# Kernel tuning notes

Measured on AMD Instinct MI355X. Metric: run time of the kernel, lower is better.

## Reference

```python
import jax, jax.numpy as jnp
import numpy as np

HIDDEN = 1024
HEADS = 16


def rotate_half(x):
    x1, x2 = jnp.split(x, 2, axis=-1)
    return jnp.concatenate((-x2, x1), axis=-1)


def rope_tables(seq_len, dim):
    inv_freq = 1.0 / 10000 ** (jnp.arange(0, dim, 2, dtype=jnp.float32) / dim)
    t = jnp.arange(seq_len, dtype=jnp.float32)
    freqs = jnp.outer(t, inv_freq)
    emb = jnp.concatenate((freqs, freqs), axis=-1)  # [S, dim]
    return jnp.cos(emb), jnp.sin(emb)


def setup_inputs() -> dict:
    key = jax.random.key(0)
    ks = jax.random.split(key, 10)
    B, S, D = 2, 2048, HIDDEN
    scale = 1.0 / np.sqrt(D)
    inp = {
        "inputs": jax.random.normal(ks[0], (B, S, D), jnp.float32),
        "context": jax.random.normal(ks[1], (B, S, D), jnp.float32),
        "Wq": jax.random.normal(ks[2], (D, D), jnp.float32) * scale,
        "bq": jnp.zeros((D,), jnp.float32),
        "Wk": jax.random.normal(ks[3], (D, D), jnp.float32) * scale,
        "bk": jnp.zeros((D,), jnp.float32),
        "Wv": jax.random.normal(ks[4], (D, D), jnp.float32) * scale,
        "bv": jnp.zeros((D,), jnp.float32),
        "Wo": jax.random.normal(ks[5], (D, D), jnp.float32) * scale,
        "bo": jnp.zeros((D,), jnp.float32),
    }
    return inp


def reference(inputs, context, Wq, bq, Wk, bk, Wv, bv, Wo, bo):
    B, S, D = inputs.shape
    H = HEADS
    hd = D // H

    q = inputs @ Wq + bq          # [B,S,D]
    k = context @ Wk + bk
    v = context @ Wv + bv

    # RoPE applied over the FULL hidden dim, pre-head-split (faithful to source).
    cos, sin = rope_tables(S, D)  # [S,D]
    # source indexes [0] after broadcasting with [1,1,S,D] tables -> effectively same values
    q = q * cos + rotate_half(q) * sin
    k = k * cos + rotate_half(k) * sin

    q = q.reshape(B, S, H, hd)
    k = k.reshape(B, S, H, hd)
    v = v.reshape(B, S, H, hd)

    # Faithful: NO transpose before attention; matmul contracts last dims of
    # q [B,S,H,hd] with k^T [B,S,hd,H] -> scores [B,S,H,H]
    scores = jnp.einsum('bshd,btd->bsht', q, jnp.zeros((1, 1, 1))) if False else None
    scores = jnp.matmul(q, jnp.swapaxes(k, -2, -1)) / jnp.sqrt(jnp.float32(hd))  # [B,S,H,H]
    attn = jax.nn.softmax(scores, axis=-1)
    ctx = jnp.matmul(attn, v)     # [B,S,H,hd]

    # source: transpose(0,2,1,3) then reshape back to (B,S,D)
    ctx = ctx.transpose(0, 2, 1, 3).reshape(B, S, D)
    out = ctx @ Wo + bo
    return out, attn
```

## Files before the change

kernel.cpp:

```cpp
#include <hip/hip_runtime.h>
#include <hip/hip_bf16.h>
#include <cstdint>

typedef __attribute__((ext_vector_type(8))) short short8;
typedef __attribute__((ext_vector_type(4))) float f32x4;
typedef __attribute__((ext_vector_type(4))) float float4v;
typedef __attribute__((ext_vector_type(4))) unsigned short us4;

#define HD 1024
#define SEQ 2048

__device__ __forceinline__ unsigned short f2bf(float f) {
  uint32_t u = __builtin_bit_cast(uint32_t, f);
  return (unsigned short)((u + 0x7FFFu + ((u >> 16) & 1u)) >> 16);
}
__device__ __forceinline__ float bf2f(unsigned short s) {
  return __builtin_bit_cast(float, (uint32_t)s << 16);
}

__device__ __forceinline__ void gload16(const unsigned short* g, unsigned short* l) {
  __builtin_amdgcn_global_load_lds(
      (const __attribute__((address_space(1))) void*)g,
      (__attribute__((address_space(3))) void*)l, 16, 0, 0);
}

__global__ __launch_bounds__(256) void prep(
    const float* __restrict__ X, const float* __restrict__ Y,
    const float* __restrict__ w0, const float* __restrict__ w1,
    const float* __restrict__ w2, const float* __restrict__ w3,
    unsigned short* __restrict__ Xh, unsigned short* __restrict__ Yh,
    unsigned short* __restrict__ wt) {
  __shared__ float tile[32][33];
  int bx = blockIdx.x;
  int tid = threadIdx.x;
  if (bx < 4096) {
    const float* src = (bx >= 2048) ? Y : X;
    unsigned short* oh = (bx >= 2048) ? Yh : Xh;
    int i0 = (bx & 2047) * 512 + tid;
#pragma unroll
    for (int r = 0; r < 2; ++r) {
      int i = i0 + r * 256;
      float4v v = ((const float4v*)src)[i];
      us4 h;
#pragma unroll
      for (int j = 0; j < 4; ++j) h[j] = f2bf(v[j]);
      ((us4*)oh)[i] = h;
    }
  } else {
    int t = bx - 4096;
    int z = t >> 10;
    int rem = t & 1023;
    int bxx = rem & 31, byy = rem >> 5;
    const float* in = (z == 0) ? w0 : (z == 1) ? w1 : (z == 2) ? w2 : w3;
    unsigned short* oh = wt + (size_t)z * 1024 * 1024;
    int tx = tid & 31, ty = tid >> 5;
    int x = bxx * 32 + tx;
    int y0 = byy * 32;
    for (int i = ty; i < 32; i += 8)
      tile[i][tx] = in[(size_t)(y0 + i) * HD + x];
    __syncthreads();
    int x2 = y0 + tx;
    int y2 = bxx * 32;
    for (int i = ty; i < 32; i += 8)
      oh[(size_t)(y2 + i) * HD + x2] = f2bf(tile[tx][i]);
  }
}

__global__ __launch_bounds__(256, 3) void gemm_qkv(
    const unsigned short* __restrict__ Ih, const unsigned short* __restrict__ Ch,
    const unsigned short* __restrict__ wt,
    const float* __restrict__ bq, const float* __restrict__ bk, const float* __restrict__ bv,
    unsigned short* __restrict__ qo, unsigned short* __restrict__ ko,
    unsigned short* __restrict__ vo) {
  __shared__ __align__(16) unsigned short lds[2][128][64];
  const int K = HD, N = HD;
  const size_t P = (size_t)1024 * 1024;
  int z  = blockIdx.z;
  const unsigned short* Ah = z ? Ch : Ih;
  const unsigned short* Bth = wt + (size_t)z * P;
  const float* bias = (z == 0) ? bq : (z == 1) ? bk : bv;
  unsigned short* C = (z == 0) ? qo : (z == 1) ? ko : vo;

  int m0 = blockIdx.x * 128;
  int n0 = blockIdx.y * 128;
  int tid  = threadIdx.x;
  int lane = tid & 63;
  int w    = tid >> 6;
  int quad = lane >> 4;
  int l16  = lane & 15;
  int wm = (w >> 1) * 64;
  int wn = (w & 1) * 64;

  int ro = lane >> 3;
  int sl = lane & 7;
  int ge = sl ^ (ro >> 1);
  int go = ge ^ 4;
  const unsigned short* spA_e = Ah  + (size_t)(m0 + ro) * K + ge * 8;
  const unsigned short* spA_o = Ah  + (size_t)(m0 + ro) * K + go * 8;
  const unsigned short* spB_e = Bth + (size_t)(n0 + ro) * K + ge * 8;
  const unsigned short* spB_o = Bth + (size_t)(n0 + ro) * K + go * 8;

  f32x4 acc[4][4];
#pragma unroll
  for (int t = 0; t < 4; ++t)
#pragma unroll
    for (int u = 0; u < 4; ++u) acc[t][u] = (f32x4){0.f, 0.f, 0.f, 0.f};

  for (int k0 = 0; k0 < K; k0 += 64) {
    __syncthreads();
#pragma unroll
    for (int i = 0; i < 4; ++i) {
      int seg = w + i * 4;
      const unsigned short* pa = (seg & 1) ? spA_o : spA_e;
      const unsigned short* pb = (seg & 1) ? spB_o : spB_e;
      gload16(pa + (size_t)seg * 8 * K + k0, &lds[0][seg * 8][0]);
      gload16(pb + (size_t)seg * 8 * K + k0, &lds[1][seg * 8][0]);
    }
    __syncthreads();

#pragma unroll
    for (int j = 0; j < 2; ++j) {
      int sl8 = (((j << 2) | quad) ^ (l16 >> 1)) * 8;
      short8 ah[4], bh[4];
#pragma unroll
      for (int t = 0; t < 4; ++t)
        ah[t] = *(const short8*)&lds[0][wm + t * 16 + l16][sl8];
#pragma unroll
      for (int u = 0; u < 4; ++u)
        bh[u] = *(const short8*)&lds[1][wn + u * 16 + l16][sl8];
#pragma unroll
      for (int t = 0; t < 4; ++t)
#pragma unroll
        for (int u = 0; u < 4; ++u)
          acc[t][u] = __builtin_amdgcn_mfma_f32_16x16x32_bf16(ah[t], bh[u], acc[t][u], 0, 0, 0);
    }
  }

#pragma unroll
  for (int t = 0; t < 4; ++t) {
    int row = m0 + wm + t * 16 + quad * 4;
#pragma unroll
    for (int u = 0; u < 4; ++u) {
      int col = n0 + wn + u * 16 + l16;
      float bvv = bias[col];
#pragma unroll
      for (int i = 0; i < 4; ++i)
        C[(size_t)(row + i) * N + col] = f2bf(acc[t][u][i] + bvv);
    }
  }
}

__global__ __launch_bounds__(256, 3) void gemm_o(
    const unsigned short* __restrict__ Ah, const unsigned short* __restrict__ Bth,
    const float* __restrict__ bias, float* __restrict__ C) {
  __shared__ __align__(16) unsigned short ldsA[128][64];
  __shared__ __align__(16) unsigned short ldsB[64][64];
  const int K = HD, N = HD;
  int m0 = blockIdx.x * 128;
  int n0 = blockIdx.y * 64;
  int tid  = threadIdx.x;
  int lane = tid & 63;
  int w    = tid >> 6;
  int quad = lane >> 4;
  int l16  = lane & 15;
  int wm = (w >> 1) * 64;
  int wn = (w & 1) * 32;

  int ro = lane >> 3;
  int sl = lane & 7;
  int ge = sl ^ (ro >> 1);
  int go = ge ^ 4;
  const unsigned short* spA_e = Ah  + (size_t)(m0 + ro) * K + ge * 8;
  const unsigned short* spA_o = Ah  + (size_t)(m0 + ro) * K + go * 8;
  const unsigned short* spB_e = Bth + (size_t)(n0 + ro) * K + ge * 8;
  const unsigned short* spB_o = Bth + (size_t)(n0 + ro) * K + go * 8;

  f32x4 acc[4][2];
#pragma unroll
  for (int t = 0; t < 4; ++t)
#pragma unroll
    for (int u = 0; u < 2; ++u) acc[t][u] = (f32x4){0.f, 0.f, 0.f, 0.f};

  for (int k0 = 0; k0 < K; k0 += 64) {
    __syncthreads();
#pragma unroll
    for (int i = 0; i < 4; ++i) {
      int seg = w + i * 4;
      const unsigned short* pa = (seg & 1) ? spA_o : spA_e;
      gload16(pa + (size_t)seg * 8 * K + k0, &ldsA[seg * 8][0]);
    }
#pragma unroll
    for (int i = 0; i < 2; ++i) {
      int seg = w + i * 4;
      const unsigned short* pb = (seg & 1) ? spB_o : spB_e;
      gload16(pb + (size_t)seg * 8 * K + k0, &ldsB[seg * 8][0]);
    }
    __syncthreads();

#pragma unroll
    for (int j = 0; j < 2; ++j) {
      int sl8 = (((j << 2) | quad) ^ (l16 >> 1)) * 8;
      short8 ah[4], bh[2];
#pragma unroll
      for (int t = 0; t < 4; ++t)
        ah[t] = *(const short8*)&ldsA[wm + t * 16 + l16][sl8];
#pragma unroll
      for (int u = 0; u < 2; ++u)
        bh[u] = *(const short8*)&ldsB[wn + u * 16 + l16][sl8];
#pragma unroll
      for (int t = 0; t < 4; ++t)
#pragma unroll
        for (int u = 0; u < 2; ++u)
          acc[t][u] = __builtin_amdgcn_mfma_f32_16x16x32_bf16(ah[t], bh[u], acc[t][u], 0, 0, 0);
    }
  }

#pragma unroll
  for (int t = 0; t < 4; ++t) {
    int row = m0 + wm + t * 16 + quad * 4;
#pragma unroll
    for (int u = 0; u < 2; ++u) {
      int col = n0 + wn + u * 16 + l16;
      float bvv = bias[col];
#pragma unroll
      for (int i = 0; i < 4; ++i)
        C[(size_t)(row + i) * N + col] = acc[t][u][i] + bvv;
    }
  }
}

__global__ __launch_bounds__(256) void attn_rope_k(
    const unsigned short* __restrict__ q, const unsigned short* __restrict__ kk,
    const unsigned short* __restrict__ v,
    float* __restrict__ attn_out, unsigned short* __restrict__ ctx_h) {
  __shared__ __align__(16) unsigned short vs[4][16][64];
  int tid = threadIdx.x;
  int lane = tid & 63;
  int w = tid >> 6;
  int m = blockIdx.x * 4 + w;
  int s = m & (SEQ - 1);
  int b = m >> 11;
  int l16 = lane & 15;
  int quad = lane >> 4;

  {
    unsigned short* dst = &vs[w][0][0];
    const unsigned short* src = v + (size_t)m * HD;
    gload16(src + lane * 8, dst);
    gload16(src + 512 + lane * 8, dst + 512);
  }

  const unsigned short* qrow = q + (size_t)m * HD + l16 * 64 + quad * 8;
  const unsigned short* krow = kk + (size_t)m * HD + l16 * 64 + quad * 8;
  float qf[2][8], kf[2][8];
#pragma unroll
  for (int j = 0; j < 2; ++j) {
    short8 qv = *(const short8*)(qrow + j * 32);
    short8 kv = *(const short8*)(krow + j * 32);
#pragma unroll
    for (int e = 0; e < 8; ++e) {
      qf[j][e] = bf2f((unsigned short)qv[e]);
      kf[j][e] = bf2f((unsigned short)kv[e]);
    }
  }

  const float C = 0.025952563241307517f;
  const float I2PI = 0.15915494309189535f;
  float fs = (float)s;
  int pbase = (l16 & 7) * 64 + quad * 8;
  bool hi = (l16 & 8) != 0;
#pragma unroll
  for (int j = 0; j < 2; ++j) {
#pragma unroll
    for (int e = 0; e < 8; ++e) {
      int p = pbase + j * 32 + e;
      float f = exp2f(-(float)p * C);
      float rev = fs * f * I2PI;
      rev -= floorf(rev);
      float sv = __builtin_amdgcn_sinf(rev);
      float cv = __builtin_amdgcn_cosf(rev);
      float pq = __shfl_xor(qf[j][e], 8);
      float pk = __shfl_xor(kf[j][e], 8);
      float sg = hi ? sv : -sv;
      qf[j][e] = qf[j][e] * cv + pq * sg;
      kf[j][e] = kf[j][e] * cv + pk * sg;
    }
  }

  short8 qh[2], kh[2];
#pragma unroll
  for (int j = 0; j < 2; ++j)
#pragma unroll
    for (int e = 0; e < 8; ++e) {
      qh[j][e] = (short)f2bf(qf[j][e]);
      kh[j][e] = (short)f2bf(kf[j][e]);
    }

  f32x4 acc = (f32x4){0.f, 0.f, 0.f, 0.f};
  acc = __builtin_amdgcn_mfma_f32_16x16x32_bf16(kh[0], qh[0], acc, 0, 0, 0);
  acc = __builtin_amdgcn_mfma_f32_16x16x32_bf16(kh[1], qh[1], acc, 0, 0, 0);

  float sc[4];
#pragma unroll
  for (int i = 0; i < 4; ++i) sc[i] = acc[i] * 0.125f;
  float mx = fmaxf(fmaxf(sc[0], sc[1]), fmaxf(sc[2], sc[3]));
  mx = fmaxf(mx, __shfl_xor(mx, 16));
  mx = fmaxf(mx, __shfl_xor(mx, 32));
  float ee[4];
  float sum = 0.f;
#pragma unroll
  for (int i = 0; i < 4; ++i) { ee[i] = expf(sc[i] - mx); sum += ee[i]; }
  sum += __shfl_xor(sum, 16);
  sum += __shfl_xor(sum, 32);
  float inv = 1.0f / sum;
  f32x4 av;
#pragma unroll
  for (int i = 0; i < 4; ++i) av[i] = ee[i] * inv;

  *(f32x4*)(attn_out + (size_t)m * 256 + l16 * 16 + quad * 4) = av;

  float sh[4][4];
#pragma unroll
  for (int i = 0; i < 4; ++i) {
    sh[0][i] = av[i];
    sh[1][i] = __shfl_xor(av[i], 16);
    sh[2][i] = __shfl_xor(av[i], 32);
    sh[3][i] = __shfl_xor(sh[1][i], 32);
  }

  asm volatile("s_waitcnt vmcnt(0)" ::: "memory");
  float c[16];
#pragma unroll
  for (int d = 0; d < 16; ++d) c[d] = 0.f;
  const unsigned short(*vw)[64] = vs[w];
  int d0 = quad * 16;
#pragma unroll
  for (int qq = 0; qq < 4; ++qq) {
    int tb = ((quad ^ qq) << 2);
#pragma unroll
    for (int i = 0; i < 4; ++i) {
      int t = tb + i;
      float aval = sh[qq][i];
      short8 v0 = *(const short8*)&vw[t][d0];
      short8 v1 = *(const short8*)&vw[t][d0 + 8];
#pragma unroll
      for (int d = 0; d < 8; ++d) {
        c[d]     = fmaf(aval, bf2f((unsigned short)v0[d]), c[d]);
        c[8 + d] = fmaf(aval, bf2f((unsigned short)v1[d]), c[8 + d]);
      }
    }
  }

  int row = b * SEQ + l16 * 128 + (s >> 4);
  int col = (s & 15) * 64 + d0;
  unsigned short* cp = ctx_h + (size_t)row * HD + col;
  short8 o0, o1;
#pragma unroll
  for (int d = 0; d < 8; ++d) {
    o0[d] = (short)f2bf(c[d]);
    o1[d] = (short)f2bf(c[8 + d]);
  }
  *(short8*)cp = o0;
  *((short8*)(cp + 8)) = o1;
}

extern "C" void kernel_launch(void* const* d_in, const int* in_sizes, int n_in,
                              void* d_out, int out_size, void* d_ws, size_t ws_size,
                              hipStream_t stream) {
  const float* inputs  = (const float*)d_in[0];
  const float* context = (const float*)d_in[1];
  const float* Wq = (const float*)d_in[2];
  const float* bq = (const float*)d_in[3];
  const float* Wk = (const float*)d_in[4];
  const float* bk = (const float*)d_in[5];
  const float* Wv = (const float*)d_in[6];
  const float* bv = (const float*)d_in[7];
  const float* Wo = (const float*)d_in[8];
  const float* bo = (const float*)d_in[9];

  float* out  = (float*)d_out;
  float* attn = out + (size_t)4096 * 1024;

  const size_t MB = 1ull << 20;
  char* wsb = (char*)d_ws;
  unsigned short* q  = (unsigned short*)(wsb + 0 * MB);
  unsigned short* k  = (unsigned short*)(wsb + 8 * MB);
  unsigned short* v  = (unsigned short*)(wsb + 16 * MB);
  unsigned short* wt = (unsigned short*)(wsb + 24 * MB);
  unsigned short* Ih = (unsigned short*)(wsb + 32 * MB);
  unsigned short* Ch = (unsigned short*)(wsb + 40 * MB);
  unsigned short* ctxh = Ih;

  prep<<<8192, 256, 0, stream>>>(inputs, context, Wq, Wk, Wv, Wo, Ih, Ch, wt);

  gemm_qkv<<<dim3(32, 8, 3), 256, 0, stream>>>(Ih, Ch, wt, bq, bk, bv, q, k, v);

  attn_rope_k<<<1024, 256, 0, stream>>>(q, k, v, attn, ctxh);

  const size_t P = (size_t)1024 * 1024;
  gemm_o<<<dim3(32, 16), 256, 0, stream>>>(ctxh, wt + 3 * P, bo, out);
}
```

Baseline: 161.7 us.

## Rewrite QKV GEMM as 256x256 tile, 8-wave, double-buffered pipelined kernel

Replaces the 128x128 single-buffered QKV GEMM with a 256x256-tile, 512-thread kernel. It double-buffers A and B in LDS, interleaves async global-to-LDS loads with MFMA quadrants, and uses explicit waitcnt, barriers and setprio to overlap memory with compute. The larger tile raises data reuse per block. The grid shrinks to 192 blocks on a 256-CU part, so some CUs sit idle, and the heavy manual scheduling adds risk of hazards.

```diff
diff --git a/kernel.cpp b/kernel.cpp
--- a/kernel.cpp
+++ b/kernel.cpp
@@ -66,88 +66,147 @@
   }
 }
 
-__global__ __launch_bounds__(256, 3) void gemm_qkv(
+__global__ __launch_bounds__(512, 2) void gemm_qkv8(
     const unsigned short* __restrict__ Ih, const unsigned short* __restrict__ Ch,
     const unsigned short* __restrict__ wt,
     const float* __restrict__ bq, const float* __restrict__ bk, const float* __restrict__ bv,
     unsigned short* __restrict__ qo, unsigned short* __restrict__ ko,
     unsigned short* __restrict__ vo) {
-  __shared__ __align__(16) unsigned short lds[2][128][64];
-  const int K = HD, N = HD;
-  const size_t P = (size_t)1024 * 1024;
-  int z  = blockIdx.z;
-  const unsigned short* Ah = z ? Ch : Ih;
-  const unsigned short* Bth = wt + (size_t)z * P;
+  __shared__ __align__(16) unsigned short ldsA[2][256][64];
+  __shared__ __align__(16) unsigned short ldsB[2][256][64];
+  const int N = HD;
+  int z = blockIdx.z;
+  const unsigned short* Ap = z ? Ch : Ih;
+  const unsigned short* Bp = wt + (size_t)z * 1024 * 1024;
   const float* bias = (z == 0) ? bq : (z == 1) ? bk : bv;
   unsigned short* C = (z == 0) ? qo : (z == 1) ? ko : vo;
 
-  int m0 = blockIdx.x * 128;
-  int n0 = blockIdx.y * 128;
-  int tid  = threadIdx.x;
+  int m0 = blockIdx.x * 256;
+  int n0 = blockIdx.y * 256;
+  int tid = threadIdx.x;
   int lane = tid & 63;
-  int w    = tid >> 6;
+  int w = tid >> 6;
   int quad = lane >> 4;
-  int l16  = lane & 15;
-  int wm = (w >> 1) * 64;
-  int wn = (w & 1) * 64;
-
-  int ro = lane >> 3;
-  int sl = lane & 7;
-  int ge = sl ^ (ro >> 1);
-  int go = ge ^ 4;
-  const unsigned short* spA_e = Ah  + (size_t)(m0 + ro) * K + ge * 8;
-  const unsigned short* spA_o = Ah  + (size_t)(m0 + ro) * K + go * 8;
-  const unsigned short* spB_e = Bth + (size_t)(n0 + ro) * K + ge * 8;
-  const unsigned short* spB_o = Bth + (size_t)(n0 + ro) * K + go * 8;
-
-  f32x4 acc[4][4];
-#pragma unroll
-  for (int t = 0; t < 4; ++t)
-#pragma unroll
-    for (int u = 0; u < 4; ++u) acc[t][u] = (f32x4){0.f, 0.f, 0.f, 0.f};
-
-  for (int k0 = 0; k0 < K; k0 += 64) {
-    __syncthreads();
-#pragma unroll
-    for (int i = 0; i < 4; ++i) {
-      int seg = w + i * 4;
-      const unsigned short* pa = (seg & 1) ? spA_o : spA_e;
-      const unsigned short* pb = (seg & 1) ? spB_o : spB_e;
-      gload16(pa + (size_t)seg * 8 * K + k0, &lds[0][seg * 8][0]);
-      gload16(pb + (size_t)seg * 8 * K + k0, &lds[1][seg * 8][0]);
-    }
-    __syncthreads();
-
-#pragma unroll
-    for (int j = 0; j < 2; ++j) {
-      int sl8 = (((j << 2) | quad) ^ (l16 >> 1)) * 8;
-      short8 ah[4], bh[4];
-#pragma unroll
-      for (int t = 0; t < 4; ++t)
-        ah[t] = *(const short8*)&lds[0][wm + t * 16 + l16][sl8];
-#pragma unroll
-      for (int u = 0; u < 4; ++u)
-        bh[u] = *(const short8*)&lds[1][wn + u * 16 + l16][sl8];
-#pragma unroll
-      for (int t = 0; t < 4; ++t)
-#pragma unroll
-        for (int u = 0; u < 4; ++u)
-          acc[t][u] = __builtin_amdgcn_mfma_f32_16x16x32_bf16(ah[t], bh[u], acc[t][u], 0, 0, 0);
-    }
-  }
-
-#pragma unroll
-  for (int t = 0; t < 4; ++t) {
-    int row = m0 + wm + t * 16 + quad * 4;
-#pragma unroll
-    for (int u = 0; u < 4; ++u) {
-      int col = n0 + wn + u * 16 + l16;
-      float bvv = bias[col];
-#pragma unroll
-      for (int i = 0; i < 4; ++i)
-        C[(size_t)(row + i) * N + col] = f2bf(acc[t][u][i] + bvv);
-    }
-  }
+  int l16 = lane & 15;
+  int wm = (w >> 2) * 64;
+  int wn = (w & 3) * 32;
+
+  int r0 = tid >> 3;
+  int sl = tid & 7;
+  int chs = sl ^ ((r0 >> 1) & 7);
+  const unsigned short* pAs = Ap + (size_t)(m0 + r0) * HD + chs * 8;
+  const unsigned short* pBs = Bp + (size_t)(n0 + r0) * HD + chs * 8;
+
+  int xsw = (l16 >> 1) & 7;
+  int c0 = (quad ^ xsw) * 8;
+  int c1 = c0 ^ 32;
+
+  f32x4 acc[2][2][4][2];
+#pragma unroll
+  for (int a = 0; a < 2; ++a)
+#pragma unroll
+    for (int b = 0; b < 2; ++b)
+#pragma unroll
+      for (int ta = 0; ta < 4; ++ta)
+#pragma unroll
+        for (int ub = 0; ub < 2; ++ub) acc[a][b][ta][ub] = (f32x4){0.f, 0.f, 0.f, 0.f};
+
+  short8 ah[4][2];
+  short8 bh[2][2][2];
+
+#define STAGE_A8(par, h, kt) { if ((kt) < 16) { \
+    const unsigned short* sp_ = pAs + (size_t)((h) * 128) * HD + (size_t)(kt) * 64; \
+    unsigned short* dp_ = (unsigned short*)ldsA[par] + (h) * 8192 + w * 512; \
+    gload16(sp_, dp_); \
+    gload16(sp_ + (size_t)64 * HD, dp_ + 4096); } }
+#define STAGE_B8(par, h, kt) { if ((kt) < 16) { \
+    const unsigned short* sp_ = pBs + (size_t)((h) * 128) * HD + (size_t)(kt) * 64; \
+    unsigned short* dp_ = (unsigned short*)ldsB[par] + (h) * 8192 + w * 512; \
+    gload16(sp_, dp_); \
+    gload16(sp_ + (size_t)64 * HD, dp_ + 4096); } }
+#define LDA8(par, a) { \
+    _Pragma("unroll") for (int ta = 0; ta < 4; ++ta) { \
+      const unsigned short* rp_ = &ldsA[par][(a) * 128 + wm + ta * 16 + l16][0]; \
+      ah[ta][0] = *(const short8*)(rp_ + c0); \
+      ah[ta][1] = *(const short8*)(rp_ + c1); } }
+#define LDB4(par, b) { \
+    _Pragma("unroll") for (int ub = 0; ub < 2; ++ub) { \
+      const unsigned short* rp_ = &ldsB[par][(b) * 128 + wn + ub * 16 + l16][0]; \
+      bh[(b)][ub][0] = *(const short8*)(rp_ + c0); \
+      bh[(b)][ub][1] = *(const short8*)(rp_ + c1); } }
+#define MMQ(a, b) { \
+    __builtin_amdgcn_s_setprio(1); \
+    _Pragma("unroll") for (int ta = 0; ta < 4; ++ta) \
+      _Pragma("unroll") for (int ub = 0; ub < 2; ++ub) { \
+        acc[(a)][(b)][ta][ub] = __builtin_amdgcn_mfma_f32_16x16x32_bf16(ah[ta][0], bh[(b)][ub][0], acc[(a)][(b)][ta][ub], 0, 0, 0); \
+        acc[(a)][(b)][ta][ub] = __builtin_amdgcn_mfma_f32_16x16x32_bf16(ah[ta][1], bh[(b)][ub][1], acc[(a)][(b)][ta][ub], 0, 0, 0); } \
+    __builtin_amdgcn_s_setprio(0); }
+#define PSYNC() { __builtin_amdgcn_s_barrier(); \
+    asm volatile("s_waitcnt lgkmcnt(0)" ::: "memory"); \
+    __builtin_amdgcn_sched_barrier(0); }
+#define PEND() { __builtin_amdgcn_sched_barrier(0); __builtin_amdgcn_s_barrier(); }
+
+  STAGE_A8(0, 0, 0); STAGE_B8(0, 0, 0); STAGE_A8(0, 1, 0); STAGE_B8(0, 1, 0);
+  STAGE_A8(1, 0, 1); STAGE_B8(1, 0, 1); STAGE_A8(1, 1, 1);
+  asm volatile("s_waitcnt vmcnt(6)" ::: "memory");
+  __builtin_amdgcn_s_barrier();
+
+  for (int it = 0; it < 8; ++it) {
+    int base = it * 2;
+    LDA8(0, 0); LDB4(0, 0);
+    STAGE_B8(1, 1, base + 1);
+    PSYNC(); MMQ(0, 0); PEND();
+    LDB4(0, 1);
+    STAGE_A8(0, 0, base + 2);
+    PSYNC(); MMQ(0, 1); PEND();
+    LDA8(0, 1);
+    STAGE_B8(0, 0, base + 2);
+    PSYNC(); MMQ(1, 0); PEND();
+    STAGE_A8(0, 1, base + 2);
+    PSYNC(); MMQ(1, 1);
+    __builtin_amdgcn_sched_barrier(0);
+    if (it == 7) { asm volatile("s_waitcnt vmcnt(0)" ::: "memory"); }
+    else         { asm volatile("s_waitcnt vmcnt(6)" ::: "memory"); }
+    __builtin_amdgcn_s_barrier();
+    LDA8(1, 0); LDB4(1, 0);
+    STAGE_B8(0, 1, base + 2);
+    PSYNC(); MMQ(0, 0); PEND();
+    LDB4(1, 1);
+    STAGE_A8(1, 0, base + 3);
+    PSYNC(); MMQ(0, 1); PEND();
+    LDA8(1, 1);
+    STAGE_B8(1, 0, base + 3);
+    PSYNC(); MMQ(1, 0); PEND();
+    STAGE_A8(1, 1, base + 3);
+    PSYNC(); MMQ(1, 1);
+    __builtin_amdgcn_sched_barrier(0);
+    asm volatile("s_waitcnt vmcnt(6)" ::: "memory");
+    __builtin_amdgcn_s_barrier();
+  }
+
+#pragma unroll
+  for (int a = 0; a < 2; ++a)
+#pragma unroll
+    for (int b = 0; b < 2; ++b)
+#pragma unroll
+      for (int ta = 0; ta < 4; ++ta) {
+        int row = m0 + a * 128 + wm + ta * 16 + quad * 4;
+#pragma unroll
+        for (int ub = 0; ub < 2; ++ub) {
+          int col = n0 + b * 128 + wn + ub * 16 + l16;
+          float bvv = bias[col];
+#pragma unroll
+          for (int i = 0; i < 4; ++i)
+            C[(size_t)(row + i) * N + col] = f2bf(acc[a][b][ta][ub][i] + bvv);
+        }
+      }
+#undef STAGE_A8
+#undef STAGE_B8
+#undef LDA8
+#undef LDB4
+#undef MMQ
+#undef PSYNC
+#undef PEND
 }
 
 __global__ __launch_bounds__(256, 3) void gemm_o(
@@ -393,7 +452,7 @@
 
   prep<<<8192, 256, 0, stream>>>(inputs, context, Wq, Wk, Wv, Wo, Ih, Ch, wt);
 
-  gemm_qkv<<<dim3(32, 8, 3), 256, 0, stream>>>(Ih, Ch, wt, bq, bk, bv, q, k, v);
+  gemm_qkv8<<<dim3(16, 4, 3), 512, 0, stream>>>(Ih, Ch, wt, bq, bk, bv, q, k, v);
 
   attn_rope_k<<<1024, 256, 0, stream>>>(q, k, v, attn, ctxh);
 
```

New measurement: 167.5 us. 1.04x slower.
